# Optimization experiments

Measured on AMD Instinct MI355X. Metric: run time of the kernel, lower is better.

The kernel has to match this reference:

```python
import jax, jax.numpy as jnp
import numpy as np

B, T, C, N = 4, 12, 64, 10000
H = 64            # d_inner (GRU hidden)
L = 2             # num_layers
NE = 2000         # number of static hyperedges
NNZ = 80000       # incidence list length
TOPK = 10         # HGCNADP_topk
DE = 16           # HGCNADP_embed_dims
RATE = 0.5        # hyperedge_rate (blend static vs adaptive)


def setup_inputs() -> dict:
    key = jax.random.key(0)
    ks = jax.random.split(key, 10)
    scale = 0.05
    x = jax.random.normal(ks[0], (B, T, C, N), jnp.float32)
    node_idx = jax.random.randint(ks[1], (NNZ,), 0, N, jnp.int32)
    edge_idx = jax.random.randint(ks[2], (NNZ,), 0, NE, jnp.int32)
    hyperedge_index = jnp.stack([node_idx, edge_idx])  # (2, NNZ)
    node_embs = jax.random.normal(ks[3], (L, N, DE), jnp.float32) * 0.1
    W_zr = jax.random.normal(ks[4], (L, C + H, 2 * H), jnp.float32) * scale
    b_zr = jnp.zeros((L, 2 * H), jnp.float32)
    W_c = jax.random.normal(ks[5], (L, C + H, H), jnp.float32) * scale
    b_c = jnp.zeros((L, H), jnp.float32)
    W_out = jax.random.normal(ks[6], (L, H, C), jnp.float32) * scale
    b_out = jnp.zeros((L, C), jnp.float32)
    return {"x": x, "hyperedge_index": hyperedge_index, "node_embs": node_embs,
            "W_zr": W_zr, "b_zr": b_zr, "W_c": W_c, "b_c": b_c,
            "W_out": W_out, "b_out": b_out}


def reference(x, hyperedge_index, node_embs, W_zr, b_zr, W_c, b_c, W_out, b_out):
    # x: (B, T, C, N). Dropout is identity (eval mode).
    node_idx = hyperedge_index[0]
    edge_idx = hyperedge_index[1]
    edge_deg = jnp.zeros((NE,), x.dtype).at[edge_idx].add(1.0)
    inv_e = 1.0 / jnp.maximum(edge_deg, 1.0)
    node_deg = jnp.zeros((N,), x.dtype).at[node_idx].add(1.0)
    inv_n = 1.0 / jnp.maximum(node_deg, 1.0)

    def conv(f, topk_idx, topk_w):
        # f: (B, N, D). Static hypergraph pass: node -> hyperedge -> node.
        msg = jnp.take(f, node_idx, axis=1)                       # (B, NNZ, D)
        eagg = jnp.zeros((f.shape[0], NE, f.shape[2]), f.dtype).at[:, edge_idx].add(msg)
        eagg = eagg * inv_e[None, :, None]                        # (B, NE, D)
        stat = jnp.zeros_like(f).at[:, node_idx].add(jnp.take(eagg, edge_idx, axis=1))
        stat = stat * inv_n[None, :, None]                        # (B, N, D)
        # Adaptive top-k hyperedge aggregation (softmax-weighted neighbor sum).
        adp = jnp.einsum('bnkd,nk->bnd', jnp.take(f, topk_idx, axis=1), topk_w)
        return RATE * stat + (1.0 - RATE) * adp

    out = x
    for l in range(L):
        xl = out.transpose(0, 1, 3, 2)                            # (B, T, N, C)
        E = node_embs[l]
        scores = jax.nn.relu(E @ E.T)                             # (N, N)
        vals, idx = jax.lax.top_k(scores, TOPK)                   # (N, K)
        w = jax.nn.softmax(vals, axis=-1)
        Wz, bz = W_zr[l], b_zr[l]
        Wc_, bc_ = W_c[l], b_c[l]
        Wo, bo = W_out[l], b_out[l]

        def step(h, x_t):
            zr = jax.nn.sigmoid(conv(jnp.concatenate([x_t, h], -1), idx, w) @ Wz + bz)
            z, r = jnp.split(zr, 2, axis=-1)
            c = jnp.tanh(conv(jnp.concatenate([x_t, r * h], -1), idx, w) @ Wc_ + bc_)
            h_new = z * h + (1.0 - z) * c
            return h_new, h_new @ Wo + bo

        h0 = jnp.zeros((out.shape[0], N, H), x.dtype)
        _, ys = jax.lax.scan(step, h0, xl.transpose(1, 0, 2, 3))  # ys: (T, B, N, C)
        out = out + ys.transpose(1, 0, 3, 2)                      # residual, back to (B,T,C,N)
    return out
```

## Files before the change

kernel.cpp:

```cpp
#include <hip/hip_runtime.h>
#include <hip/hip_fp16.h>
#include <cstdio>

#define BB 4
#define TT 12
#define CC 64
#define NN 10000
#define HH 64
#define LL 2
#define NEDGE 2000
#define NNZT 80000
#define KTOP 10
#define DEMB 16
#define BT (BB*TT)

typedef long long ll;
typedef unsigned long long u64;
typedef unsigned int u32;
typedef unsigned short ushort;

typedef short bf16x8 __attribute__((ext_vector_type(8)));
typedef float f32x4 __attribute__((ext_vector_type(4)));

__device__ __forceinline__ void up8(const uint4 v, float* f) {
  const __half2* p = reinterpret_cast<const __half2*>(&v);
  float2 t0 = __half22float2(p[0]);
  float2 t1 = __half22float2(p[1]);
  float2 t2 = __half22float2(p[2]);
  float2 t3 = __half22float2(p[3]);
  f[0]=t0.x; f[1]=t0.y; f[2]=t1.x; f[3]=t1.y;
  f[4]=t2.x; f[5]=t2.y; f[6]=t3.x; f[7]=t3.y;
}
__device__ __forceinline__ uint4 pk8(const float* f) {
  __half2 h0 = __floats2half2_rn(f[0], f[1]);
  __half2 h1 = __floats2half2_rn(f[2], f[3]);
  __half2 h2 = __floats2half2_rn(f[4], f[5]);
  __half2 h3 = __floats2half2_rn(f[6], f[7]);
  uint4 r;
  r.x = *reinterpret_cast<unsigned*>(&h0);
  r.y = *reinterpret_cast<unsigned*>(&h1);
  r.z = *reinterpret_cast<unsigned*>(&h2);
  r.w = *reinterpret_cast<unsigned*>(&h3);
  return r;
}
__device__ __forceinline__ ushort f2bf(float x) {
  u32 u = __float_as_uint(x);
  u32 r = u + 0x7FFFu + ((u >> 16) & 1u);
  return (ushort)(r >> 16);
}
__device__ __forceinline__ uint4 pk8bf(const float* f) {
  uint4 r;
  r.x = (u32)f2bf(f[0]) | ((u32)f2bf(f[1])<<16);
  r.y = (u32)f2bf(f[2]) | ((u32)f2bf(f[3])<<16);
  r.z = (u32)f2bf(f[4]) | ((u32)f2bf(f[5])<<16);
  r.w = (u32)f2bf(f[6]) | ((u32)f2bf(f[7])<<16);
  return r;
}

__global__ void deg_kernel(const int* __restrict__ nidx, const int* __restrict__ eidx,
                           int* __restrict__ ndeg, int* __restrict__ edeg) {
  int i = blockIdx.x*256 + threadIdx.x;
  if (i < NNZT) { atomicAdd(&ndeg[nidx[i]],1); atomicAdd(&edeg[eidx[i]],1); }
}

__global__ void exscan_kernel(const int* __restrict__ cnt, int* __restrict__ off, int n) {
  __shared__ int part[256];
  int tid = threadIdx.x;
  int chunk = (n + 255)/256;
  int lo = tid*chunk, hi = min(lo+chunk, n);
  int s = 0;
  for (int i=lo; i<hi; ++i) s += cnt[i];
  part[tid]=s; __syncthreads();
  if (tid==0){ int acc=0; for(int i=0;i<256;++i){int v=part[i];part[i]=acc;acc+=v;} off[n]=acc; }
  __syncthreads();
  int acc = part[tid];
  for (int i=lo; i<hi; ++i){ off[i]=acc; acc+=cnt[i]; }
}

__global__ void fill_csr_kernel(const int* __restrict__ nidx, const int* __restrict__ eidx,
                                const int* __restrict__ noff, const int* __restrict__ eoff,
                                int* __restrict__ ncur, int* __restrict__ ecur,
                                int* __restrict__ node_edges, int* __restrict__ edge_nodes) {
  int i = blockIdx.x*256 + threadIdx.x;
  if (i >= NNZT) return;
  int n = nidx[i], e = eidx[i];
  int pn = atomicAdd(&ncur[n],1);
  node_edges[noff[n]+pn] = e;
  int pe = atomicAdd(&ecur[e],1);
  edge_nodes[eoff[e]+pe] = n;
}

__global__ void invdeg_kernel(const int* __restrict__ ndeg, const int* __restrict__ edeg,
                              float* __restrict__ inv_n, float* __restrict__ inv_e) {
  int i = blockIdx.x*256+threadIdx.x;
  if (i < NN) inv_n[i] = 1.0f/fmaxf((float)ndeg[i],1.0f);
  if (i < NEDGE) inv_e[i] = 1.0f/fmaxf((float)edeg[i],1.0f);
}

__global__ void prep_w_kernel(const float* __restrict__ W_zr, const float* __restrict__ W_c,
                              const float* __restrict__ W_o,
                              short* __restrict__ Wz_swb, short* __restrict__ Wc_swb,
                              short* __restrict__ Wo_swb) {
  int l = blockIdx.y;
  const float* Wz = W_zr + (size_t)l*128*128;
  const float* Wc = W_c  + (size_t)l*128*64;
  const float* Wo = W_o  + (size_t)l*64*64;
  short* Wz_sw = Wz_swb + (size_t)l*16384;
  short* Wc_sw = Wc_swb + (size_t)l*8192;
  short* Wo_sw = Wo_swb + (size_t)l*4096;
  int idx = blockIdx.x*256 + threadIdx.x;
  if (idx < 16384) {
    int i = idx&7, lane = (idx>>3)&63, kk = (idx>>9)&3, tc = idx>>11;
    int k = kk*32 + (lane>>4)*8 + i, col = tc*16 + (lane&15);
    Wz_sw[idx] = (short)f2bf(Wz[k*128+col]);
  }
  if (idx < 8192) {
    int i = idx&7, lane = (idx>>3)&63, kk = (idx>>9)&3, tc = idx>>11;
    int k = kk*32 + (lane>>4)*8 + i, col = tc*16 + (lane&15);
    Wc_sw[idx] = (short)f2bf(Wc[k*64+col]);
  }
  if (idx < 4096) {
    int i = idx&7, lane = (idx>>3)&63, kk = (idx>>9)&1, tc = idx>>10;
    int k = kk*32 + (lane>>4)*8 + i, col = tc*16 + (lane&15);
    Wo_sw[idx] = (short)f2bf(Wo[k*64+col]);
  }
}

__device__ __forceinline__ u64 sortstep(u64 X, int j, bool dir, int lane) {
  u64 p = __shfl_xor(X, j);
  bool lower = ((lane & j) == 0);
  bool keep_min = (dir == lower);
  bool xlt = (X < p);
  u64 mn = xlt ? X : p;
  u64 mx = xlt ? p : X;
  return keep_min ? mn : mx;
}

__device__ __forceinline__ void reselect(u64* bq, u64& thr, int& cnt, int lane) {
  int tot = 10 + cnt;
  u64 A = (lane < tot)      ? bq[lane]      : 0ull;
  u64 B = (lane + 64 < tot) ? bq[lane + 64] : 0ull;
  for (int k = 2; k <= 32; k <<= 1) {
    for (int j = k >> 1; j >= 1; j >>= 1) {
      bool dir = ((lane & k) == 0);
      A = sortstep(A, j, dir, lane);
      B = sortstep(B, j, dir, lane);
    }
  }
  for (int j = 32; j >= 1; j >>= 1) {
    A = sortstep(A, j, true,  lane);
    B = sortstep(B, j, false, lane);
  }
  {
    bool lt = (A < B);
    u64 mn = lt ? A : B, mx = lt ? B : A;
    A = mn; B = mx;
  }
  for (int j = 32; j >= 1; j >>= 1) {
    A = sortstep(A, j, true, lane);
    B = sortstep(B, j, true, lane);
  }
  if (lane >= 54) bq[63 - lane] = B;
  thr = __shfl(B, 54);
  cnt = 0;
}

__global__ void __launch_bounds__(256) topk_kernel(const float* __restrict__ embs,
                                                   int* __restrict__ tk_idx_b,
                                                   float* __restrict__ tk_w_b) {
  __shared__ u64 buf[16][128];
  const float* E = embs + (ll)blockIdx.y*NN*DEMB;
  int* tk_idx = tk_idx_b + (ll)blockIdx.y*NN*KTOP;
  float* tk_w = tk_w_b + (ll)blockIdx.y*NN*KTOP;
  int tid = threadIdx.x;
  int wv = tid >> 6, lane = tid & 63;
  int qbase = blockIdx.x*16 + wv*4;
  const float4* E4 = (const float4*)E;
  float4 q[4][4];
  #pragma unroll
  for (int u=0;u<4;++u) {
    int n = qbase + u;
    #pragma unroll
    for (int j=0;j<4;++j) q[u][j] = E4[(ll)n*4 + j];
  }
  u64 thr[4] = {0,0,0,0};
  int cnt[4] = {0,0,0,0};
  buf[tid>>4][tid&15] = 0ull;
  for (int cb=0; cb<NN; cb+=64) {
    int cand = cb + lane;
    bool valid = (cand < NN);
    int ca = valid ? cand : 0;
    float4 a0 = E4[(ll)ca*4], a1 = E4[(ll)ca*4+1], a2 = E4[(ll)ca*4+2], a3 = E4[(ll)ca*4+3];
    u64 low = (u64)(0x00FFFFFFu - (unsigned)cand);
    u64 key[4];
    #pragma unroll
    for (int u=0;u<4;++u) {
      float dot = q[u][0].x*a0.x + q[u][0].y*a0.y + q[u][0].z*a0.z + q[u][0].w*a0.w
                + q[u][1].x*a1.x + q[u][1].y*a1.y + q[u][1].z*a1.z + q[u][1].w*a1.w
                + q[u][2].x*a2.x + q[u][2].y*a2.y + q[u][2].z*a2.z + q[u][2].w*a2.w
                + q[u][3].x*a3.x + q[u][3].y*a3.y + q[u][3].z*a3.z + q[u][3].w*a3.w;
      float s = fmaxf(dot, 0.f);
      u64 kk = ((u64)__float_as_uint(s) << 32) | low;
      key[u] = valid ? kk : 0ull;
    }
    #pragma unroll
    for (int u=0;u<4;++u) {
      u64 mask = __ballot(key[u] > thr[u]);
      if (mask) {
        if (key[u] > thr[u]) {
          int myofs = (int)__popcll(mask & ((1ull<<lane)-1ull));
          buf[wv*4+u][10 + cnt[u] + myofs] = key[u];
        }
        cnt[u] += (int)__popcll(mask);
        if (cnt[u] >= 40) reselect(&buf[wv*4+u][0], thr[u], cnt[u], lane);
      }
    }
  }
  #pragma unroll
  for (int u=0;u<4;++u) {
    u64* bq = &buf[wv*4+u][0];
    if (cnt[u] > 0) reselect(bq, thr[u], cnt[u], lane);
    u64 k10 = (lane < 10) ? bq[lane] : 0ull;
    float v = __uint_as_float((unsigned)(k10 >> 32));
    int idx = 0x00FFFFFF - (int)(k10 & 0xFFFFFFFFull);
    float v0 = __shfl(v, 0);
    float e = (lane < 10) ? expf(v - v0) : 0.f;
    float s = e;
    for (int o=1;o<16;o<<=1) s += __shfl_xor(s, o);
    if (lane < 10) {
      int n = qbase + u;
      tk_w[n*KTOP + lane] = e / s;
      tk_idx[n*KTOP + lane] = idx;
    }
  }
}

__global__ void transpose_kernel(const float* __restrict__ src, __half* __restrict__ dst) {
  __shared__ float tile[32][33];
  int bt = blockIdx.z;
  int n0 = blockIdx.x*32, c0 = blockIdx.y*32;
  for (int i=threadIdx.y; i<32; i+=8) {
    int c = c0+i, nn = n0+threadIdx.x;
    tile[i][threadIdx.x] = (nn<NN)? src[((ll)bt*CC + c)*NN + nn] : 0.0f;
  }
  __syncthreads();
  for (int i=threadIdx.y; i<32; i+=8) {
    int nn = n0+i, c = c0+threadIdx.x;
    if (nn<NN) dst[((ll)bt*NN+nn)*64 + c] = __float2half_rn(tile[threadIdx.x][i]);
  }
}

__global__ void __launch_bounds__(256) edge_agg_kernel(
    const uint4* __restrict__ f8, uint4* __restrict__ eagg8,
    const int* __restrict__ eoff, const int* __restrict__ enodes,
    const float* __restrict__ inv_e) {
  __shared__ int en_s[1088];
  __shared__ int jo_s[17];
  int tid = threadIdx.x;
  int e0 = blockIdx.x*16;
  int s = blockIdx.y;
  if (tid < 17) jo_s[tid] = eoff[e0 + tid];
  __syncthreads();
  int jb0 = jo_s[0], cnt = jo_s[16] - jb0;
  bool stg = (cnt <= 1088);
  if (stg) for (int i = tid; i < cnt; i += 256) en_s[i] = enodes[jb0 + i];
  __syncthreads();
  int esub = tid>>4;
  int e = e0 + esub;
  int hsel = (tid>>3)&1;
  int lane8 = tid&7;
  int j0 = jo_s[esub] - jb0, j1 = jo_s[esub+1] - jb0;
  const uint4* fb = f8 + (ll)s*NN*8;
  float acc[8] = {0,0,0,0,0,0,0,0};
  for (int j = j0 + hsel; j < j1; j += 2) {
    int node = stg ? en_s[j] : enodes[jb0+j];
    float t[8]; up8(fb[(ll)node*8 + lane8], t);
    #pragma unroll
    for (int q=0;q<8;++q) acc[q] += t[q];
  }
  #pragma unroll
  for (int q=0;q<8;++q) acc[q] += __shfl_xor(acc[q], 8);
  if (hsel == 0) {
    float sc = inv_e[e];
    #pragma unroll
    for (int q=0;q<8;++q) acc[q] *= sc;
    eagg8[((ll)s*NEDGE+e)*8 + lane8] = pk8(acc);
  }
}

__global__ void __launch_bounds__(256) conv_x_kernel(
    const uint4* __restrict__ xt8, const uint4* __restrict__ eagg8,
    const int* __restrict__ noff, const int* __restrict__ nedges,
    const float* __restrict__ inv_n,
    const int* __restrict__ tk_idx, const float* __restrict__ tk_w,
    uint4* __restrict__ cx8) {
  __shared__ int tki_s[32][KTOP];
  __shared__ float tkw_s[32][KTOP];
  __shared__ int ne_s[640];
  __shared__ int no_s[33];
  int tid = threadIdx.x; int s = blockIdx.y; int n0 = blockIdx.x*32;
  if (tid < 33) no_s[tid] = noff[min(n0 + tid, NN)];
  for (int i=tid; i<32*KTOP; i+=256) {
    int r=i/KTOP, k=i%KTOP; int n = n0+r;
    tki_s[r][k] = (n<NN)? tk_idx[n*KTOP+k] : 0;
    tkw_s[r][k] = (n<NN)? tk_w[n*KTOP+k] : 0.f;
  }
  __syncthreads();
  int jb0 = no_s[0], cnt = no_s[32] - jb0;
  bool stg = (cnt <= 640);
  if (stg) for (int i=tid; i<cnt; i+=256) ne_s[i] = nedges[jb0+i];
  __syncthreads();
  int row = tid>>3, lane8 = tid&7;
  int n = n0 + row;
  if (n >= NN) return;
  float stv[8] = {0,0,0,0,0,0,0,0};
  const uint4* eb = eagg8 + (ll)s*NEDGE*8;
  int j0 = no_s[row] - jb0, j1 = no_s[row+1] - jb0;
  for (int j=j0;j<j1;++j) {
    int eidx = stg ? ne_s[j] : nedges[jb0+j];
    float t[8]; up8(eb[(ll)eidx*8 + lane8], t);
    #pragma unroll
    for (int q=0;q<8;++q) stv[q] += t[q];
  }
  float sc = 0.5f*inv_n[n];
  float adv[8] = {0,0,0,0,0,0,0,0};
  const uint4* xb = xt8 + (ll)s*NN*8;
  #pragma unroll
  for (int k=0;k<KTOP;++k) {
    float w = tkw_s[row][k];
    float t[8]; up8(xb[(ll)tki_s[row][k]*8 + lane8], t);
    #pragma unroll
    for (int q=0;q<8;++q) adv[q] += w*t[q];
  }
  float r8[8];
  #pragma unroll
  for (int q=0;q<8;++q) r8[q] = sc*stv[q] + 0.5f*adv[q];
  cx8[((ll)s*NN+n)*8+lane8] = pk8(r8);
}

__global__ void __launch_bounds__(256) step0_kernel(
    const uint4* __restrict__ cx8,
    const short* __restrict__ Wz_sw, const float* __restrict__ bz,
    const short* __restrict__ Wc_sw, const float* __restrict__ bc,
    const short* __restrict__ Wo_sw, const float* __restrict__ bo,
    __half* __restrict__ h, float* __restrict__ out) {
  __shared__ __align__(16) short in_bf[32][72];
  __shared__ __align__(16) short hn[32][72];
  __shared__ __align__(16) float yt[64][36];
  int tid = threadIdx.x;
  int b = blockIdx.y; int n0 = blockIdx.x*32;
  int bt = b*TT;
  {
    int row = tid>>3, lane8 = tid&7;
    int n = n0 + row;
    float cxv[8] = {0,0,0,0,0,0,0,0};
    if (n < NN) up8(cx8[((ll)bt*NN + n)*8 + lane8], cxv);
    *(uint4*)&in_bf[row][lane8*8] = pk8bf(cxv);
  }
  __syncthreads();
  int wv = tid>>6, lane = tid&63;
  int m = lane&15, g = lane>>4;
  #pragma unroll
  for (int q=0;q<2;++q) {
    int T = wv + 4*q;
    int tr = T>>2, tc = T&3;
    f32x4 az = {0.f,0.f,0.f,0.f};
    f32x4 ac = {0.f,0.f,0.f,0.f};
    #pragma unroll
    for (int kk=0;kk<2;++kk) {
      bf16x8 a = *(const bf16x8*)&in_bf[tr*16 + m][kk*32 + g*8];
      bf16x8 bwz = *(const bf16x8*)&Wz_sw[((tc*4+kk)*64 + lane)*8];
      bf16x8 bwc = *(const bf16x8*)&Wc_sw[((tc*4+kk)*64 + lane)*8];
      az = __builtin_amdgcn_mfma_f32_16x16x32_bf16(a, bwz, az, 0, 0, 0);
      ac = __builtin_amdgcn_mfma_f32_16x16x32_bf16(a, bwc, ac, 0, 0, 0);
    }
    int col = tc*16 + m;
    float bzv = bz[col], bcv = bc[col];
    #pragma unroll
    for (int r=0;r<4;++r) {
      int row = tr*16 + g*4 + r;
      int n = n0 + row;
      float z = 1.0f/(1.0f+expf(-(az[r]+bzv)));
      float cval = tanhf(ac[r]+bcv);
      float hnew = (1.0f-z)*cval;
      if (n < NN) h[((ll)b*NN+n)*64+col] = __float2half_rn(hnew);
      hn[row][col] = (short)f2bf(hnew);
    }
  }
  __syncthreads();
  #pragma unroll
  for (int q=0;q<2;++q) {
    int T = wv + 4*q;
    int tr = T>>2, tc = T&3;
    f32x4 acc = {0.f,0.f,0.f,0.f};
    #pragma unroll
    for (int kk=0;kk<2;++kk) {
      bf16x8 a = *(const bf16x8*)&hn[tr*16 + m][kk*32 + g*8];
      bf16x8 bw = *(const bf16x8*)&Wo_sw[((tc*2+kk)*64 + lane)*8];
      acc = __builtin_amdgcn_mfma_f32_16x16x32_bf16(a, bw, acc, 0, 0, 0);
    }
    int col = tc*16 + m;
    float bias = bo[col];
    #pragma unroll
    for (int r=0;r<4;++r) {
      int row = tr*16 + g*4 + r;
      yt[col][row] = acc[r] + bias;
    }
  }
  __syncthreads();
  #pragma unroll
  for (int kk=0;kk<2;++kk) {
    int slot = tid + kk*256;
    int col = slot>>3, q = slot&7;
    int n = n0 + q*4;
    if (n < NN) {
      float4 y = *(const float4*)&yt[col][q*4];
      float4* dst = (float4*)&out[((ll)bt*64+col)*NN + n];
      float4 cur = *dst;
      cur.x += y.x; cur.y += y.y; cur.z += y.z; cur.w += y.w;
      *dst = cur;
    }
  }
}

__global__ void __launch_bounds__(256) step_zr_kernel(
    const uint4* __restrict__ h8, const uint4* __restrict__ cx8,
    const uint4* __restrict__ eagg8,
    const short* __restrict__ Wz_sw, const float* __restrict__ bz,
    const int* __restrict__ noff, const int* __restrict__ nedges,
    const float* __restrict__ inv_n,
    const int* __restrict__ tk_idx, const float* __restrict__ tk_w,
    const __half* __restrict__ hs,
    __half* __restrict__ rh, __half* __restrict__ zout, int t) {
  __shared__ __align__(16) short in_bf[32][136];
  __shared__ int tki_s[32][KTOP];
  __shared__ float tkw_s[32][KTOP];
  __shared__ int ne_s[640];
  __shared__ int no_s[33];
  int tid = threadIdx.x;
  int b = blockIdx.y; int n0 = blockIdx.x*32;
  int bt = b*TT + t;
  if (tid < 33) no_s[tid] = noff[min(n0 + tid, NN)];
  for (int i=tid; i<32*KTOP; i+=256) {
    int r=i/KTOP, k=i%KTOP; int n=n0+r;
    tki_s[r][k] = (n<NN)? tk_idx[n*KTOP+k] : 0;
    tkw_s[r][k] = (n<NN)? tk_w[n*KTOP+k] : 0.f;
  }
  __syncthreads();
  int jb0 = no_s[0], ecnt = no_s[32] - jb0;
  bool stg = (ecnt <= 640);
  if (stg) for (int i=tid; i<ecnt; i+=256) ne_s[i] = nedges[jb0+i];
  __syncthreads();
  {
    int row = tid>>3, lane8 = tid&7;
    int n = n0 + row;
    float cxv[8] = {0,0,0,0,0,0,0,0};
    float chv[8] = {0,0,0,0,0,0,0,0};
    if (n < NN) {
      up8(cx8[((ll)bt*NN + n)*8 + lane8], cxv);
      float stv[8] = {0,0,0,0,0,0,0,0};
      int j0 = no_s[row] - jb0, j1 = no_s[row+1] - jb0;
      const uint4* eb = eagg8 + (ll)b*NEDGE*8;
      for (int j=j0;j<j1;++j) {
        int eidx = stg ? ne_s[j] : nedges[jb0+j];
        float t8[8]; up8(eb[(ll)eidx*8 + lane8], t8);
        #pragma unroll
        for (int q=0;q<8;++q) stv[q] += t8[q];
      }
      float sc = 0.5f*inv_n[n];
      const uint4* hb = h8 + (ll)b*NN*8;
      float adv[8] = {0,0,0,0,0,0,0,0};
      #pragma unroll
      for (int k=0;k<KTOP;++k) {
        float w = tkw_s[row][k];
        float t8[8]; up8(hb[(ll)tki_s[row][k]*8 + lane8], t8);
        #pragma unroll
        for (int q=0;q<8;++q) adv[q] += w*t8[q];
      }
      #pragma unroll
      for (int q=0;q<8;++q) chv[q] = sc*stv[q] + 0.5f*adv[q];
    }
    *(uint4*)&in_bf[row][lane8*8]    = pk8bf(cxv);
    *(uint4*)&in_bf[row][64+lane8*8] = pk8bf(chv);
  }
  __syncthreads();
  int wv = tid>>6, lane = tid&63;
  int m = lane&15, g = lane>>4;
  #pragma unroll
  for (int q=0;q<4;++q) {
    int T = wv*4 + q;
    int tr = T>>3, tc = T&7;
    f32x4 acc = {0.f,0.f,0.f,0.f};
    #pragma unroll
    for (int kk=0;kk<4;++kk) {
      bf16x8 a = *(const bf16x8*)&in_bf[tr*16 + m][kk*32 + g*8];
      bf16x8 bf = *(const bf16x8*)&Wz_sw[((tc*4+kk)*64 + lane)*8];
      acc = __builtin_amdgcn_mfma_f32_16x16x32_bf16(a, bf, acc, 0, 0, 0);
    }
    int col = tc*16 + m;
    float bias = bz[col];
    #pragma unroll
    for (int r=0;r<4;++r) {
      int row = tr*16 + g*4 + r;
      int n = n0 + row;
      if (n < NN) {
        float v = 1.0f/(1.0f+expf(-(acc[r]+bias)));
        if (col < 64) zout[((ll)b*NN+n)*64+col] = __float2half_rn(v);
        else {
          int c = col-64;
          float hv = __half2float(hs[((ll)b*NN+n)*64+c]);
          rh[((ll)b*NN+n)*64+c] = __float2half_rn(v*hv);
        }
      }
    }
  }
}

__global__ void __launch_bounds__(256) step_hy_kernel(
    const uint4* __restrict__ rh8, const uint4* __restrict__ cx8,
    const uint4* __restrict__ eagg8,
    const short* __restrict__ Wc_sw, const float* __restrict__ bc,
    const short* __restrict__ Wo_sw, const float* __restrict__ bo,
    const int* __restrict__ noff, const int* __restrict__ nedges,
    const float* __restrict__ inv_n,
    const int* __restrict__ tk_idx, const float* __restrict__ tk_w,
    const __half* __restrict__ zbuf, __half* __restrict__ h,
    float* __restrict__ out, int t) {
  __shared__ __align__(16) short in_bf[32][136];
  __shared__ __align__(16) short hn[32][72];
  __shared__ __align__(16) float yt[64][36];
  __shared__ int tki_s[32][KTOP];
  __shared__ float tkw_s[32][KTOP];
  __shared__ int ne_s[640];
  __shared__ int no_s[33];
  int tid = threadIdx.x;
  int b = blockIdx.y; int n0 = blockIdx.x*32;
  int bt = b*TT + t;
  if (tid < 33) no_s[tid] = noff[min(n0 + tid, NN)];
  for (int i=tid; i<32*KTOP; i+=256) {
    int r=i/KTOP, k=i%KTOP; int n=n0+r;
    tki_s[r][k] = (n<NN)? tk_idx[n*KTOP+k] : 0;
    tkw_s[r][k] = (n<NN)? tk_w[n*KTOP+k] : 0.f;
  }
  __syncthreads();
  int jb0 = no_s[0], ecnt = no_s[32] - jb0;
  bool stg = (ecnt <= 640);
  if (stg) for (int i=tid; i<ecnt; i+=256) ne_s[i] = nedges[jb0+i];
  __syncthreads();
  {
    int row = tid>>3, lane8 = tid&7;
    int n = n0 + row;
    float cxv[8] = {0,0,0,0,0,0,0,0};
    float chv[8] = {0,0,0,0,0,0,0,0};
    if (n < NN) {
      up8(cx8[((ll)bt*NN + n)*8 + lane8], cxv);
      float stv[8] = {0,0,0,0,0,0,0,0};
      int j0 = no_s[row] - jb0, j1 = no_s[row+1] - jb0;
      const uint4* eb = eagg8 + (ll)b*NEDGE*8;
      for (int j=j0;j<j1;++j) {
        int eidx = stg ? ne_s[j] : nedges[jb0+j];
        float t8[8]; up8(eb[(ll)eidx*8 + lane8], t8);
        #pragma unroll
        for (int q=0;q<8;++q) stv[q] += t8[q];
      }
      float sc = 0.5f*inv_n[n];
      const uint4* rb = rh8 + (ll)b*NN*8;
      float adv[8] = {0,0,0,0,0,0,0,0};
      #pragma unroll
      for (int k=0;k<KTOP;++k) {
        float w = tkw_s[row][k];
        float t8[8]; up8(rb[(ll)tki_s[row][k]*8 + lane8], t8);
        #pragma unroll
        for (int q=0;q<8;++q) adv[q] += w*t8[q];
      }
      #pragma unroll
      for (int q=0;q<8;++q) chv[q] = sc*stv[q] + 0.5f*adv[q];
    }
    *(uint4*)&in_bf[row][lane8*8]    = pk8bf(cxv);
    *(uint4*)&in_bf[row][64+lane8*8] = pk8bf(chv);
  }
  __syncthreads();
  int wv = tid>>6, lane = tid&63;
  int m = lane&15, g = lane>>4;
  #pragma unroll
  for (int q=0;q<2;++q) {
    int T = wv + 4*q;
    int tr = T>>2, tc = T&3;
    f32x4 acc = {0.f,0.f,0.f,0.f};
    #pragma unroll
    for (int kk=0;kk<4;++kk) {
      bf16x8 a = *(const bf16x8*)&in_bf[tr*16 + m][kk*32 + g*8];
      bf16x8 bf = *(const bf16x8*)&Wc_sw[((tc*4+kk)*64 + lane)*8];
      acc = __builtin_amdgcn_mfma_f32_16x16x32_bf16(a, bf, acc, 0, 0, 0);
    }
    int col = tc*16 + m;
    float bias = bc[col];
    #pragma unroll
    for (int r=0;r<4;++r) {
      int row = tr*16 + g*4 + r;
      int n = n0 + row;
      float hnew = 0.0f;
      if (n < NN) {
        float cval = tanhf(acc[r]+bias);
        float z = __half2float(zbuf[((ll)b*NN+n)*64+col]);
        float hv = __half2float(h[((ll)b*NN+n)*64+col]);
        hnew = z*hv + (1.0f-z)*cval;
        h[((ll)b*NN+n)*64+col] = __float2half_rn(hnew);
      }
      hn[row][col] = (short)f2bf(hnew);
    }
  }
  __syncthreads();
  #pragma unroll
  for (int q=0;q<2;++q) {
    int T = wv + 4*q;
    int tr = T>>2, tc = T&3;
    f32x4 acc = {0.f,0.f,0.f,0.f};
    #pragma unroll
    for (int kk=0;kk<2;++kk) {
      bf16x8 a = *(const bf16x8*)&hn[tr*16 + m][kk*32 + g*8];
      bf16x8 bf = *(const bf16x8*)&Wo_sw[((tc*2+kk)*64 + lane)*8];
      acc = __builtin_amdgcn_mfma_f32_16x16x32_bf16(a, bf, acc, 0, 0, 0);
    }
    int col = tc*16 + m;
    float bias = bo[col];
    #pragma unroll
    for (int r=0;r<4;++r) {
      int row = tr*16 + g*4 + r;
      yt[col][row] = acc[r] + bias;
    }
  }
  __syncthreads();
  #pragma unroll
  for (int kk=0;kk<2;++kk) {
    int slot = tid + kk*256;
    int col = slot>>3, q = slot&7;
    int n = n0 + q*4;
    if (n < NN) {
      float4 y = *(const float4*)&yt[col][q*4];
      float4* dst = (float4*)&out[((ll)bt*64+col)*NN + n];
      float4 cur = *dst;
      cur.x += y.x; cur.y += y.y; cur.z += y.z; cur.w += y.w;
      *dst = cur;
    }
  }
}

extern "C" void kernel_launch(void* const* d_in, const int* in_sizes, int n_in,
                              void* d_out, int out_size, void* d_ws, size_t ws_size,
                              hipStream_t stream) {
  const float* x    = (const float*)d_in[0];
  const int*  hidx  = (const int*)d_in[1];
  const float* embs = (const float*)d_in[2];
  const float* W_zr = (const float*)d_in[3];
  const float* b_zr = (const float*)d_in[4];
  const float* W_c  = (const float*)d_in[5];
  const float* b_c  = (const float*)d_in[6];
  const float* W_out= (const float*)d_in[7];
  const float* b_out= (const float*)d_in[8];
  const int* node_idx = hidx;
  const int* edge_idx = hidx + NNZT;

  char* ws = (char*)d_ws;
  size_t off = 0;
  auto alloc = [&](size_t bytes) -> void* {
    void* p = ws + off; off += (bytes + 255) & ~(size_t)255; return p;
  };
  __half* xt    = (__half*)alloc((size_t)BT*NN*64*2);
  __half* cx    = (__half*)alloc((size_t)BT*NN*64*2);
  __half* eaggx = (__half*)alloc((size_t)BT*NEDGE*64*2);
  __half* eaggh = (__half*)alloc((size_t)BB*NEDGE*64*2);
  __half* hbuf  = (__half*)alloc((size_t)BB*NN*64*2);
  __half* rhbuf = (__half*)alloc((size_t)BB*NN*64*2);
  __half* zbuf  = (__half*)alloc((size_t)BB*NN*64*2);
  short* Wz_sw = (short*)alloc((size_t)LL*16384*2);
  short* Wc_sw = (short*)alloc((size_t)LL*8192*2);
  short* Wo_sw = (short*)alloc((size_t)LL*4096*2);
  float* tkw   = (float*)alloc((size_t)LL*NN*KTOP*4);
  float* inv_e = (float*)alloc(NEDGE*4);
  float* inv_n = (float*)alloc(NN*4);
  int* tki     = (int*)alloc((size_t)LL*NN*KTOP*4);
  int* ndeg    = (int*)alloc(NN*4);
  int* edeg    = (int*)alloc(NEDGE*4);
  int* noff    = (int*)alloc((NN+1)*4);
  int* eoff    = (int*)alloc((NEDGE+1)*4);
  int* ncur    = (int*)alloc(NN*4);
  int* ecur    = (int*)alloc(NEDGE*4);
  int* nedges  = (int*)alloc(NNZT*4);
  int* enodes  = (int*)alloc(NNZT*4);
  if (off > ws_size) {
    fprintf(stderr, "kernel_launch: ws too small, need %zu have %zu\n", off, ws_size);
    return;
  }

  hipMemcpyAsync(d_out, x, (size_t)BB*TT*CC*NN*4, hipMemcpyDeviceToDevice, stream);

  hipMemsetAsync(ndeg, 0, NN*4, stream);
  hipMemsetAsync(edeg, 0, NEDGE*4, stream);
  hipMemsetAsync(ncur, 0, NN*4, stream);
  hipMemsetAsync(ecur, 0, NEDGE*4, stream);
  deg_kernel<<<(NNZT+255)/256,256,0,stream>>>(node_idx, edge_idx, ndeg, edeg);
  exscan_kernel<<<1,256,0,stream>>>(ndeg, noff, NN);
  exscan_kernel<<<1,256,0,stream>>>(edeg, eoff, NEDGE);
  fill_csr_kernel<<<(NNZT+255)/256,256,0,stream>>>(node_idx, edge_idx, noff, eoff,
                                                   ncur, ecur, nedges, enodes);
  invdeg_kernel<<<(NN+255)/256,256,0,stream>>>(ndeg, edeg, inv_n, inv_e);

  prep_w_kernel<<<dim3(64,LL),256,0,stream>>>(W_zr, W_c, W_out, Wz_sw, Wc_sw, Wo_sw);
  topk_kernel<<<dim3(625,LL),256,0,stream>>>(embs, tki, tkw);

  float* outp = (float*)d_out;
  for (int l=0; l<LL; ++l) {
    const short* Wzs = Wz_sw + (size_t)l*16384;
    const short* Wcs = Wc_sw + (size_t)l*8192;
    const short* Wos = Wo_sw + (size_t)l*4096;
    const float* bz = b_zr + l*128;
    const float* bc = b_c + l*64;
    const float* bo = b_out + l*64;
    const int* tkil = tki + (size_t)l*NN*KTOP;
    const float* tkwl = tkw + (size_t)l*NN*KTOP;
    transpose_kernel<<<dim3((NN+31)/32, CC/32, BT), dim3(32,8), 0, stream>>>(outp, xt);
    edge_agg_kernel<<<dim3(125, BT),256,0,stream>>>(
        (const uint4*)xt, (uint4*)eaggx, eoff, enodes, inv_e);
    conv_x_kernel<<<dim3(313, BT),256,0,stream>>>(
        (const uint4*)xt, (const uint4*)eaggx, noff, nedges, inv_n, tkil, tkwl, (uint4*)cx);
    step0_kernel<<<dim3(313, BB),256,0,stream>>>(
        (const uint4*)cx, Wzs, bz, Wcs, bc, Wos, bo, hbuf, outp);
    for (int t=1; t<TT; ++t) {
      edge_agg_kernel<<<dim3(125, BB),256,0,stream>>>(
          (const uint4*)hbuf, (uint4*)eaggh, eoff, enodes, inv_e);
      step_zr_kernel<<<dim3(313, BB),256,0,stream>>>(
          (const uint4*)hbuf, (const uint4*)cx, (const uint4*)eaggh, Wzs, bz,
          noff, nedges, inv_n, tkil, tkwl, hbuf, rhbuf, zbuf, t);
      edge_agg_kernel<<<dim3(125, BB),256,0,stream>>>(
          (const uint4*)rhbuf, (uint4*)eaggh, eoff, enodes, inv_e);
      step_hy_kernel<<<dim3(313, BB),256,0,stream>>>(
          (const uint4*)rhbuf, (const uint4*)cx, (const uint4*)eaggh, Wcs, bc, Wos, bo,
          noff, nedges, inv_n, tkil, tkwl, zbuf, hbuf, outp, t);
    }
  }
}
```

Before: 2.588 ms.

## Drop LDS staging in gather kernels, pack top-k pairs, store cx as bf16

Removes the shared-memory staging of CSR indices and top-k lists, along with their __syncthreads barriers, from edge_agg, conv_x and the step kernels. Those kernels now read indices directly from global memory and interleave top-k index and weight into an int2 array. edge_agg uses 8 edges per block with 4-way splitting, so the grid doubles. The top-k filter compares float scores before building 64-bit keys, and cx is written already packed as bf16 so the step kernels skip a convert. The cost is uncoalesced per-thread index loads and a precision change in cx from fp16 to bf16.

Result: slower. 2.700 ms (+4.3%).

```diff
diff --git a/kernel.cpp b/kernel.cpp
--- a/kernel.cpp
+++ b/kernel.cpp
@@ -166,12 +166,10 @@
 }
 
 __global__ void __launch_bounds__(256) topk_kernel(const float* __restrict__ embs,
-                                                   int* __restrict__ tk_idx_b,
-                                                   float* __restrict__ tk_w_b) {
+                                                   int2* __restrict__ tkc_b) {
   __shared__ u64 buf[16][128];
   const float* E = embs + (ll)blockIdx.y*NN*DEMB;
-  int* tk_idx = tk_idx_b + (ll)blockIdx.y*NN*KTOP;
-  float* tk_w = tk_w_b + (ll)blockIdx.y*NN*KTOP;
+  int2* tkc = tkc_b + (ll)blockIdx.y*NN*KTOP;
   int tid = threadIdx.x;
   int wv = tid >> 6, lane = tid & 63;
   int qbase = blockIdx.x*16 + wv*4;
@@ -184,6 +182,7 @@
     for (int j=0;j<4;++j) q[u][j] = E4[(ll)n*4 + j];
   }
   u64 thr[4] = {0,0,0,0};
+  float thrf[4] = {0.f,0.f,0.f,0.f};
   int cnt[4] = {0,0,0,0};
   buf[tid>>4][tid&15] = 0ull;
   for (int cb=0; cb<NN; cb+=64) {
@@ -192,7 +191,7 @@
     int ca = valid ? cand : 0;
     float4 a0 = E4[(ll)ca*4], a1 = E4[(ll)ca*4+1], a2 = E4[(ll)ca*4+2], a3 = E4[(ll)ca*4+3];
     u64 low = (u64)(0x00FFFFFFu - (unsigned)cand);
-    u64 key[4];
+    float sv[4];
     #pragma unroll
     for (int u=0;u<4;++u) {
       float dot = q[u][0].x*a0.x + q[u][0].y*a0.y + q[u][0].z*a0.z + q[u][0].w*a0.w
@@ -200,19 +199,22 @@
                 + q[u][2].x*a2.x + q[u][2].y*a2.y + q[u][2].z*a2.z + q[u][2].w*a2.w
                 + q[u][3].x*a3.x + q[u][3].y*a3.y + q[u][3].z*a3.z + q[u][3].w*a3.w;
       float s = fmaxf(dot, 0.f);
-      u64 kk = ((u64)__float_as_uint(s) << 32) | low;
-      key[u] = valid ? kk : 0ull;
+      sv[u] = valid ? s : -1.f;
     }
     #pragma unroll
     for (int u=0;u<4;++u) {
-      u64 mask = __ballot(key[u] > thr[u]);
+      u64 mask = __ballot(sv[u] >= thrf[u]);
       if (mask) {
-        if (key[u] > thr[u]) {
+        if (sv[u] >= thrf[u]) {
+          u64 key = ((u64)__float_as_uint(sv[u]) << 32) | low;
           int myofs = (int)__popcll(mask & ((1ull<<lane)-1ull));
-          buf[wv*4+u][10 + cnt[u] + myofs] = key[u];
+          buf[wv*4+u][10 + cnt[u] + myofs] = key;
         }
         cnt[u] += (int)__popcll(mask);
-        if (cnt[u] >= 40) reselect(&buf[wv*4+u][0], thr[u], cnt[u], lane);
+        if (cnt[u] >= 40) {
+          reselect(&buf[wv*4+u][0], thr[u], cnt[u], lane);
+          thrf[u] = __uint_as_float((u32)(thr[u] >> 32));
+        }
       }
     }
   }
@@ -229,8 +231,7 @@
     for (int o=1;o<16;o<<=1) s += __shfl_xor(s, o);
     if (lane < 10) {
       int n = qbase + u;
-      tk_w[n*KTOP + lane] = e / s;
-      tk_idx[n*KTOP + lane] = idx;
+      tkc[n*KTOP + lane] = make_int2(idx, __float_as_int(e / s));
     }
   }
 }
@@ -254,33 +255,24 @@
     const uint4* __restrict__ f8, uint4* __restrict__ eagg8,
     const int* __restrict__ eoff, const int* __restrict__ enodes,
     const float* __restrict__ inv_e) {
-  __shared__ int en_s[1088];
-  __shared__ int jo_s[17];
   int tid = threadIdx.x;
-  int e0 = blockIdx.x*16;
+  int e = blockIdx.x*8 + (tid>>5);
+  int sub = (tid>>3)&3;
+  int lane8 = tid&7;
   int s = blockIdx.y;
-  if (tid < 17) jo_s[tid] = eoff[e0 + tid];
-  __syncthreads();
-  int jb0 = jo_s[0], cnt = jo_s[16] - jb0;
-  bool stg = (cnt <= 1088);
-  if (stg) for (int i = tid; i < cnt; i += 256) en_s[i] = enodes[jb0 + i];
-  __syncthreads();
-  int esub = tid>>4;
-  int e = e0 + esub;
-  int hsel = (tid>>3)&1;
-  int lane8 = tid&7;
-  int j0 = jo_s[esub] - jb0, j1 = jo_s[esub+1] - jb0;
+  int j0 = eoff[e], j1 = eoff[e+1];
   const uint4* fb = f8 + (ll)s*NN*8;
   float acc[8] = {0,0,0,0,0,0,0,0};
-  for (int j = j0 + hsel; j < j1; j += 2) {
-    int node = stg ? en_s[j] : enodes[jb0+j];
-    float t[8]; up8(fb[(ll)node*8 + lane8], t);
+  for (int j = j0 + sub; j < j1; j += 4) {
+    float t[8]; up8(fb[(ll)enodes[j]*8 + lane8], t);
     #pragma unroll
     for (int q=0;q<8;++q) acc[q] += t[q];
   }
   #pragma unroll
   for (int q=0;q<8;++q) acc[q] += __shfl_xor(acc[q], 8);
-  if (hsel == 0) {
+  #pragma unroll
+  for (int q=0;q<8;++q) acc[q] += __shfl_xor(acc[q], 16);
+  if (sub == 0) {
     float sc = inv_e[e];
     #pragma unroll
     for (int q=0;q<8;++q) acc[q] *= sc;
@@ -292,50 +284,36 @@
     const uint4* __restrict__ xt8, const uint4* __restrict__ eagg8,
     const int* __restrict__ noff, const int* __restrict__ nedges,
     const float* __restrict__ inv_n,
-    const int* __restrict__ tk_idx, const float* __restrict__ tk_w,
+    const int2* __restrict__ tkc,
     uint4* __restrict__ cx8) {
-  __shared__ int tki_s[32][KTOP];
-  __shared__ float tkw_s[32][KTOP];
-  __shared__ int ne_s[640];
-  __shared__ int no_s[33];
   int tid = threadIdx.x; int s = blockIdx.y; int n0 = blockIdx.x*32;
-  if (tid < 33) no_s[tid] = noff[min(n0 + tid, NN)];
-  for (int i=tid; i<32*KTOP; i+=256) {
-    int r=i/KTOP, k=i%KTOP; int n = n0+r;
-    tki_s[r][k] = (n<NN)? tk_idx[n*KTOP+k] : 0;
-    tkw_s[r][k] = (n<NN)? tk_w[n*KTOP+k] : 0.f;
-  }
-  __syncthreads();
-  int jb0 = no_s[0], cnt = no_s[32] - jb0;
-  bool stg = (cnt <= 640);
-  if (stg) for (int i=tid; i<cnt; i+=256) ne_s[i] = nedges[jb0+i];
-  __syncthreads();
   int row = tid>>3, lane8 = tid&7;
   int n = n0 + row;
   if (n >= NN) return;
+  const int2* tp = tkc + n*KTOP;
+  const uint4* xb = xt8 + (ll)s*NN*8;
+  float adv[8] = {0,0,0,0,0,0,0,0};
+  #pragma unroll
+  for (int k=0;k<KTOP;++k) {
+    int2 p = tp[k];
+    float t[8]; up8(xb[(ll)p.x*8 + lane8], t);
+    float w = __int_as_float(p.y);
+    #pragma unroll
+    for (int q=0;q<8;++q) adv[q] += w*t[q];
+  }
+  int j0 = noff[n], j1 = noff[n+1];
   float stv[8] = {0,0,0,0,0,0,0,0};
   const uint4* eb = eagg8 + (ll)s*NEDGE*8;
-  int j0 = no_s[row] - jb0, j1 = no_s[row+1] - jb0;
   for (int j=j0;j<j1;++j) {
-    int eidx = stg ? ne_s[j] : nedges[jb0+j];
-    float t[8]; up8(eb[(ll)eidx*8 + lane8], t);
+    float t[8]; up8(eb[(ll)nedges[j]*8 + lane8], t);
     #pragma unroll
     for (int q=0;q<8;++q) stv[q] += t[q];
   }
   float sc = 0.5f*inv_n[n];
-  float adv[8] = {0,0,0,0,0,0,0,0};
-  const uint4* xb = xt8 + (ll)s*NN*8;
-  #pragma unroll
-  for (int k=0;k<KTOP;++k) {
-    float w = tkw_s[row][k];
-    float t[8]; up8(xb[(ll)tki_s[row][k]*8 + lane8], t);
-    #pragma unroll
-    for (int q=0;q<8;++q) adv[q] += w*t[q];
-  }
   float r8[8];
   #pragma unroll
   for (int q=0;q<8;++q) r8[q] = sc*stv[q] + 0.5f*adv[q];
-  cx8[((ll)s*NN+n)*8+lane8] = pk8(r8);
+  cx8[((ll)s*NN+n)*8+lane8] = pk8bf(r8);
 }
 
 __global__ void __launch_bounds__(256) step0_kernel(
@@ -353,9 +331,9 @@
   {
     int row = tid>>3, lane8 = tid&7;
     int n = n0 + row;
-    float cxv[8] = {0,0,0,0,0,0,0,0};
-    if (n < NN) up8(cx8[((ll)bt*NN + n)*8 + lane8], cxv);
-    *(uint4*)&in_bf[row][lane8*8] = pk8bf(cxv);
+    uint4 cxv4 = make_uint4(0,0,0,0);
+    if (n < NN) cxv4 = cx8[((ll)bt*NN + n)*8 + lane8];
+    *(uint4*)&in_bf[row][lane8*8] = cxv4;
   }
   __syncthreads();
   int wv = tid>>6, lane = tid&63;
@@ -429,58 +407,44 @@
     const short* __restrict__ Wz_sw, const float* __restrict__ bz,
     const int* __restrict__ noff, const int* __restrict__ nedges,
     const float* __restrict__ inv_n,
-    const int* __restrict__ tk_idx, const float* __restrict__ tk_w,
+    const int2* __restrict__ tkc,
     const __half* __restrict__ hs,
     __half* __restrict__ rh, __half* __restrict__ zout, int t) {
   __shared__ __align__(16) short in_bf[32][136];
-  __shared__ int tki_s[32][KTOP];
-  __shared__ float tkw_s[32][KTOP];
-  __shared__ int ne_s[640];
-  __shared__ int no_s[33];
   int tid = threadIdx.x;
   int b = blockIdx.y; int n0 = blockIdx.x*32;
   int bt = b*TT + t;
-  if (tid < 33) no_s[tid] = noff[min(n0 + tid, NN)];
-  for (int i=tid; i<32*KTOP; i+=256) {
-    int r=i/KTOP, k=i%KTOP; int n=n0+r;
-    tki_s[r][k] = (n<NN)? tk_idx[n*KTOP+k] : 0;
-    tkw_s[r][k] = (n<NN)? tk_w[n*KTOP+k] : 0.f;
-  }
-  __syncthreads();
-  int jb0 = no_s[0], ecnt = no_s[32] - jb0;
-  bool stg = (ecnt <= 640);
-  if (stg) for (int i=tid; i<ecnt; i+=256) ne_s[i] = nedges[jb0+i];
-  __syncthreads();
   {
     int row = tid>>3, lane8 = tid&7;
     int n = n0 + row;
-    float cxv[8] = {0,0,0,0,0,0,0,0};
+    uint4 cxv4 = make_uint4(0,0,0,0);
     float chv[8] = {0,0,0,0,0,0,0,0};
     if (n < NN) {
-      up8(cx8[((ll)bt*NN + n)*8 + lane8], cxv);
+      cxv4 = cx8[((ll)bt*NN + n)*8 + lane8];
+      const int2* tp = tkc + n*KTOP;
+      const uint4* hb = h8 + (ll)b*NN*8;
+      float adv[8] = {0,0,0,0,0,0,0,0};
+      #pragma unroll
+      for (int k=0;k<KTOP;++k) {
+        int2 p = tp[k];
+        float t8[8]; up8(hb[(ll)p.x*8 + lane8], t8);
+        float w = __int_as_float(p.y);
+        #pragma unroll
+        for (int q=0;q<8;++q) adv[q] += w*t8[q];
+      }
+      int j0 = noff[n], j1 = noff[n+1];
       float stv[8] = {0,0,0,0,0,0,0,0};
-      int j0 = no_s[row] - jb0, j1 = no_s[row+1] - jb0;
       const uint4* eb = eagg8 + (ll)b*NEDGE*8;
       for (int j=j0;j<j1;++j) {
-        int eidx = stg ? ne_s[j] : nedges[jb0+j];
-        float t8[8]; up8(eb[(ll)eidx*8 + lane8], t8);
+        float t8[8]; up8(eb[(ll)nedges[j]*8 + lane8], t8);
         #pragma unroll
         for (int q=0;q<8;++q) stv[q] += t8[q];
       }
       float sc = 0.5f*inv_n[n];
-      const uint4* hb = h8 + (ll)b*NN*8;
-      float adv[8] = {0,0,0,0,0,0,0,0};
-      #pragma unroll
-      for (int k=0;k<KTOP;++k) {
-        float w = tkw_s[row][k];
-        float t8[8]; up8(hb[(ll)tki_s[row][k]*8 + lane8], t8);
-        #pragma unroll
-        for (int q=0;q<8;++q) adv[q] += w*t8[q];
-      }
       #pragma unroll
       for (int q=0;q<8;++q) chv[q] = sc*stv[q] + 0.5f*adv[q];
     }
-    *(uint4*)&in_bf[row][lane8*8]    = pk8bf(cxv);
+    *(uint4*)&in_bf[row][lane8*8]    = cxv4;
     *(uint4*)&in_bf[row][64+lane8*8] = pk8bf(chv);
   }
   __syncthreads();
@@ -523,60 +487,46 @@
     const short* __restrict__ Wo_sw, const float* __restrict__ bo,
     const int* __restrict__ noff, const int* __restrict__ nedges,
     const float* __restrict__ inv_n,
-    const int* __restrict__ tk_idx, const float* __restrict__ tk_w,
+    const int2* __restrict__ tkc,
     const __half* __restrict__ zbuf, __half* __restrict__ h,
     float* __restrict__ out, int t) {
   __shared__ __align__(16) short in_bf[32][136];
   __shared__ __align__(16) short hn[32][72];
   __shared__ __align__(16) float yt[64][36];
-  __shared__ int tki_s[32][KTOP];
-  __shared__ float tkw_s[32][KTOP];
-  __shared__ int ne_s[640];
-  __shared__ int no_s[33];
   int tid = threadIdx.x;
   int b = blockIdx.y; int n0 = blockIdx.x*32;
   int bt = b*TT + t;
-  if (tid < 33) no_s[tid] = noff[min(n0 + tid, NN)];
-  for (int i=tid; i<32*KTOP; i+=256) {
-    int r=i/KTOP, k=i%KTOP; int n=n0+r;
-    tki_s[r][k] = (n<NN)? tk_idx[n*KTOP+k] : 0;
-    tkw_s[r][k] = (n<NN)? tk_w[n*KTOP+k] : 0.f;
-  }
-  __syncthreads();
-  int jb0 = no_s[0], ecnt = no_s[32] - jb0;
-  bool stg = (ecnt <= 640);
-  if (stg) for (int i=tid; i<ecnt; i+=256) ne_s[i] = nedges[jb0+i];
-  __syncthreads();
   {
     int row = tid>>3, lane8 = tid&7;
     int n = n0 + row;
-    float cxv[8] = {0,0,0,0,0,0,0,0};
+    uint4 cxv4 = make_uint4(0,0,0,0);
     float chv[8] = {0,0,0,0,0,0,0,0};
     if (n < NN) {
-      up8(cx8[((ll)bt*NN + n)*8 + lane8], cxv);
+      cxv4 = cx8[((ll)bt*NN + n)*8 + lane8];
+      const int2* tp = tkc + n*KTOP;
+      const uint4* rb = rh8 + (ll)b*NN*8;
+      float adv[8] = {0,0,0,0,0,0,0,0};
+      #pragma unroll
+      for (int k=0;k<KTOP;++k) {
+        int2 p = tp[k];
+        float t8[8]; up8(rb[(ll)p.x*8 + lane8], t8);
+        float w = __int_as_float(p.y);
+        #pragma unroll
+        for (int q=0;q<8;++q) adv[q] += w*t8[q];
+      }
+      int j0 = noff[n], j1 = noff[n+1];
       float stv[8] = {0,0,0,0,0,0,0,0};
-      int j0 = no_s[row] - jb0, j1 = no_s[row+1] - jb0;
       const uint4* eb = eagg8 + (ll)b*NEDGE*8;
       for (int j=j0;j<j1;++j) {
-        int eidx = stg ? ne_s[j] : nedges[jb0+j];
-        float t8[8]; up8(eb[(ll)eidx*8 + lane8], t8);
+        float t8[8]; up8(eb[(ll)nedges[j]*8 + lane8], t8);
         #pragma unroll
         for (int q=0;q<8;++q) stv[q] += t8[q];
       }
       float sc = 0.5f*inv_n[n];
-      const uint4* rb = rh8 + (ll)b*NN*8;
-      float adv[8] = {0,0,0,0,0,0,0,0};
-      #pragma unroll
-      for (int k=0;k<KTOP;++k) {
-        float w = tkw_s[row][k];
-        float t8[8]; up8(rb[(ll)tki_s[row][k]*8 + lane8], t8);
-        #pragma unroll
-        for (int q=0;q<8;++q) adv[q] += w*t8[q];
-      }
       #pragma unroll
       for (int q=0;q<8;++q) chv[q] = sc*stv[q] + 0.5f*adv[q];
     }
-    *(uint4*)&in_bf[row][lane8*8]    = pk8bf(cxv);
+    *(uint4*)&in_bf[row][lane8*8]    = cxv4;
     *(uint4*)&in_bf[row][64+lane8*8] = pk8bf(chv);
   }
   __syncthreads();
@@ -676,10 +626,9 @@
   short* Wz_sw = (short*)alloc((size_t)LL*16384*2);
   short* Wc_sw = (short*)alloc((size_t)LL*8192*2);
   short* Wo_sw = (short*)alloc((size_t)LL*4096*2);
-  float* tkw   = (float*)alloc((size_t)LL*NN*KTOP*4);
+  int2* tkc    = (int2*)alloc((size_t)LL*NN*KTOP*8);
   float* inv_e = (float*)alloc(NEDGE*4);
   float* inv_n = (float*)alloc(NN*4);
-  int* tki     = (int*)alloc((size_t)LL*NN*KTOP*4);
   int* ndeg    = (int*)alloc(NN*4);
   int* edeg    = (int*)alloc(NEDGE*4);
   int* noff    = (int*)alloc((NN+1)*4);
@@ -707,7 +656,7 @@
   invdeg_kernel<<<(NN+255)/256,256,0,stream>>>(ndeg, edeg, inv_n, inv_e);
 
   prep_w_kernel<<<dim3(64,LL),256,0,stream>>>(W_zr, W_c, W_out, Wz_sw, Wc_sw, Wo_sw);
-  topk_kernel<<<dim3(625,LL),256,0,stream>>>(embs, tki, tkw);
+  topk_kernel<<<dim3(625,LL),256,0,stream>>>(embs, tkc);
 
   float* outp = (float*)d_out;
   for (int l=0; l<LL; ++l) {
@@ -717,26 +666,25 @@
     const float* bz = b_zr + l*128;
     const float* bc = b_c + l*64;
     const float* bo = b_out + l*64;
-    const int* tkil = tki + (size_t)l*NN*KTOP;
-    const float* tkwl = tkw + (size_t)l*NN*KTOP;
+    const int2* tkcl = tkc + (size_t)l*NN*KTOP;
     transpose_kernel<<<dim3((NN+31)/32, CC/32, BT), dim3(32,8), 0, stream>>>(outp, xt);
-    edge_agg_kernel<<<dim3(125, BT),256,0,stream>>>(
+    edge_agg_kernel<<<dim3(250, BT),256,0,stream>>>(
         (const uint4*)xt, (uint4*)eaggx, eoff, enodes, inv_e);
     conv_x_kernel<<<dim3(313, BT),256,0,stream>>>(
-        (const uint4*)xt, (const uint4*)eaggx, noff, nedges, inv_n, tkil, tkwl, (uint4*)cx);
+        (const uint4*)xt, (const uint4*)eaggx, noff, nedges, inv_n, tkcl, (uint4*)cx);
     step0_kernel<<<dim3(313, BB),256,0,stream>>>(
         (const uint4*)cx, Wzs, bz, Wcs, bc, Wos, bo, hbuf, outp);
     for (int t=1; t<TT; ++t) {
-      edge_agg_kernel<<<dim3(125, BB),256,0,stream>>>(
+      edge_agg_kernel<<<dim3(250, BB),256,0,stream>>>(
           (const uint4*)hbuf, (uint4*)eaggh, eoff, enodes, inv_e);
       step_zr_kernel<<<dim3(313, BB),256,0,stream>>>(
           (const uint4*)hbuf, (const uint4*)cx, (const uint4*)eaggh, Wzs, bz,
-          noff, nedges, inv_n, tkil, tkwl, hbuf, rhbuf, zbuf, t);
-      edge_agg_kernel<<<dim3(125, BB),256,0,stream>>>(
+          noff, nedges, inv_n, tkcl, hbuf, rhbuf, zbuf, t);
+      edge_agg_kernel<<<dim3(250, BB),256,0,stream>>>(
           (const uint4*)rhbuf, (uint4*)eaggh, eoff, enodes, inv_e);
       step_hy_kernel<<<dim3(313, BB),256,0,stream>>>(
           (const uint4*)rhbuf, (const uint4*)cx, (const uint4*)eaggh, Wcs, bc, Wos, bo,
-          noff, nedges, inv_n, tkil, tkwl, zbuf, hbuf, outp, t);
-    }
-  }
-}
+          noff, nedges, inv_n, tkcl, zbuf, hbuf, outp, t);
+    }
+  }
+}
```
